# Performance work log

Measured on AMD Instinct MI355X. Metric: run time of the kernel, lower is better.

## Reference

```python
import jax, jax.numpy as jnp
import numpy as np

IMG, P, C = 224, 16, 3
D, H, MLP = 512, 8, 2048
L, NCLS = 10, 10      # budget, classes
N = (IMG // P) ** 2   # 196 patches
PD = C * P * P        # patch_dim = 768


def setup_inputs() -> dict:
    key = jax.random.key(0)
    ks = jax.random.split(key, 32)
    w = lambda k, shape: (jax.random.normal(k, shape, jnp.float32) * 0.02)
    return {
        'x': jax.random.normal(ks[0], (32, C, IMG, IMG), jnp.float32),
        'y': jax.random.randint(ks[1], (32, 1), 0, NCLS),
        'pos_emb': w(ks[2], (1, N + 1, D)),
        'cls_tok': w(ks[3], (1, 1, D)),
        'Wp': w(ks[4], (D, PD)), 'bp': jnp.zeros((D,), jnp.float32),
        'Wqkv': w(ks[5], (3 * D, D)),
        'Wo': w(ks[6], (D, D)), 'bo': jnp.zeros((D,), jnp.float32),
        'ln1_g': jnp.ones((D,), jnp.float32), 'ln1_b': jnp.zeros((D,), jnp.float32),
        'ln2_g': jnp.ones((D,), jnp.float32), 'ln2_b': jnp.zeros((D,), jnp.float32),
        'W1': w(ks[7], (MLP, D)), 'b1': jnp.zeros((MLP,), jnp.float32),
        'W2': w(ks[8], (D, MLP)), 'b2': jnp.zeros((D,), jnp.float32),
        'lnh_g': jnp.ones((D,), jnp.float32), 'lnh_b': jnp.zeros((D,), jnp.float32),
        'Wh1': w(ks[9], (MLP, D)), 'bh1': jnp.zeros((MLP,), jnp.float32),
        'Wh2': w(ks[10], (1, MLP)), 'bh2': jnp.zeros((1,), jnp.float32),
        'lnc_g': jnp.ones((D,), jnp.float32), 'lnc_b': jnp.zeros((D,), jnp.float32),
        'Wc1': w(ks[11], (MLP, D)), 'bc1': jnp.zeros((MLP,), jnp.float32),
        'Wc2': w(ks[12], (NCLS, MLP)), 'bc2': jnp.zeros((NCLS,), jnp.float32),
    }


def _ln(u, g, b):
    mu = u.mean(-1, keepdims=True)
    v = ((u - mu) ** 2).mean(-1, keepdims=True)
    return (u - mu) / jnp.sqrt(v + 1e-5) * g + b


def _gelu(u):
    return jax.nn.gelu(u, approximate=False)


def reference(x, y, pos_emb, cls_tok, Wp, bp, Wqkv, Wo, bo,
              ln1_g, ln1_b, ln2_g, ln2_b, W1, b1, W2, b2,
              lnh_g, lnh_b, Wh1, bh1, Wh2, bh2,
              lnc_g, lnc_b, Wc1, bc1, Wc2, bc2):
    b = x.shape[0]
    hp = IMG // P
    # patchify: b c (h p1) (w p2) -> b (h w) (p1 p2 c)
    xp = x.reshape(b, C, hp, P, hp, P).transpose(0, 2, 4, 3, 5, 1).reshape(b, N, PD)
    e = xp @ Wp.T + bp                                   # [b, N, D]
    z = jnp.concatenate([jnp.broadcast_to(cls_tok, (b, 1, D)), e], 1) + pos_emb[:, :N + 1]

    scale = D ** -0.5

    def attn(u):
        q, k, v = jnp.split(u @ Wqkv.T, 3, axis=-1)
        hsplit = lambda t: t.reshape(b, -1, H, D // H).transpose(0, 2, 1, 3)  # b h n d
        q, k, v = hsplit(q), hsplit(k), hsplit(v)
        a = jax.nn.softmax(jnp.einsum('bhid,bhjd->bhij', q, k) * scale, axis=-1)
        o = jnp.einsum('bhij,bhjd->bhid', a, v).transpose(0, 2, 1, 3).reshape(b, -1, D)
        return o @ Wo.T + bo

    def ff(u):
        return _gelu(u @ W1.T + b1) @ W2.T + b2

    def halt(u):
        h = _gelu(_ln(u, lnh_g, lnh_b) @ Wh1.T + bh1) @ Wh2.T + bh2  # [b, n, 1]
        return jax.nn.sigmoid(h).mean(1)[:, 0]                        # [b]

    def step(u, _):
        u = u + attn(_ln(u, ln1_g, ln1_b))
        u = u + ff(_ln(u, ln2_g, ln2_b))
        return u, (u[:, 0], halt(u))

    _, (cls_outs, halts) = jax.lax.scan(step, z, None, length=L)
    cls_outs = cls_outs.transpose(1, 0, 2)   # [b, L, D]
    halts = halts.T                          # [b, L]

    logits = _gelu(_ln(cls_outs, lnc_g, lnc_b) @ Wc1.T + bc1) @ Wc2.T + bc2  # [b, L, 10]
    logp = jax.nn.log_softmax(logits, -1)
    lab = y[:, 0]
    ce = -jnp.take_along_axis(logp, jnp.broadcast_to(lab[:, None, None], (b, L, 1)), axis=2)[..., 0]  # [b, L]

    idx = jnp.argmin(ce, axis=1) + 1                     # [b], halting step per sample
    steps = jnp.arange(L)
    mask = (steps[None, :] < idx[:, None]).astype(ce.dtype)
    denom = idx.astype(ce.dtype)
    ref_ce = (ce * mask).sum(1) / denom                  # per-sample mean over first idx steps

    # halt labels: 1 for steps < idx-1, 0 at step idx-1 (only first idx entries count)
    hl = jnp.where(steps[None, :] == (idx[:, None] - 1), 0.0, 1.0)
    p = jnp.clip(halts, 1e-7, 1.0 - 1e-7)
    bce = -(hl * jnp.log(p) + (1.0 - hl) * jnp.log1p(-p))
    halt_loss = (bce * mask).sum(1) / denom

    return ref_ce.mean() + halt_loss.mean()
```

## Files before the change

### kernel.cpp

```cpp
#include <hip/hip_runtime.h>
#include <math.h>

#define BBATCH 32
#define NTOK 197
#define NPATCH 196
#define PDIM 768
#define DDIM 512
#define NHEAD 8
#define DHEAD 64
#define MLPDIM 2048
#define NLAYER 10
#define NCLASS 10
#define MTOK (BBATCH*NTOK)
#define MPAD 6400
#define MPATCH (BBATCH*NPATCH)
#define QKVROWS (MTOK + 16)

typedef unsigned short u16;
typedef __attribute__((ext_vector_type(8))) short bf16x8;
typedef __attribute__((ext_vector_type(4))) float f32x4;

__device__ __forceinline__ float gelu_f(float x) {
    return 0.5f * x * (1.0f + erff(x * 0.70710678118654752440f));
}
__device__ __forceinline__ float bf2f(u16 u) {
    union { unsigned int i; float f; } v; v.i = ((unsigned int)u) << 16; return v.f;
}
__device__ __forceinline__ u16 f2bf(float f) {
    union { float f; unsigned int u; } v; v.f = f;
    unsigned int r = v.u + 0x7FFFu + ((v.u >> 16) & 1u);
    return (u16)(r >> 16);
}
__device__ __forceinline__ void gload_lds16(const u16* g, u16* l) {
    __builtin_amdgcn_global_load_lds((const __attribute__((address_space(1))) void*)g,
                                     (__attribute__((address_space(3))) void*)l, 16, 0, 0);
}
__device__ __forceinline__ int swz_bij(int wg, int nwg) {
    int q = nwg >> 3, r = nwg & 7, xcd = wg & 7, id8 = wg >> 3;
    return (xcd < r) ? xcd * (q + 1) + id8 : r * (q + 1) + (xcd - r) * q + id8;
}

template<int MODEA, int MODEB>
__global__ __launch_bounds__(512)
void gemm256_kernel(int nA, int colsA, int colsB,
                    const u16* __restrict__ Aa, const u16* __restrict__ Wa,
                    const float* __restrict__ biasa, void* __restrict__ outa, int Na,
                    const u16* __restrict__ Ab, const u16* __restrict__ Wb,
                    const float* __restrict__ biasb, const float* __restrict__ wh2,
                    void* __restrict__ outb, int Nb, int M)
{
    __shared__ u16 As[2][256 * 64];
    __shared__ u16 Bs[2][128 * 64];
    const int tid = threadIdx.x, lane = tid & 63, wid = tid >> 6;
    const int wr = wid >> 1, wc = wid & 1;

    const int swz = swz_bij(blockIdx.x, gridDim.x);
    int mode, m0, n0, Nn;
    const u16 *A, *W; const float* bias; void* out;
    if (swz < nA) {
        mode = MODEA; A = Aa; W = Wa; bias = biasa; out = outa; Nn = Na;
        m0 = (swz / colsA) * 256; n0 = (swz % colsA) * 128;
    } else {
        int s2 = swz - nA;
        mode = MODEB; A = Ab; W = Wb; bias = biasb; out = outb; Nn = Nb;
        m0 = (s2 / colsB) * 256; n0 = (s2 % colsB) * 128;
    }

    f32x4 acc[4][4] = {};
    const int srow = tid >> 3;
    const int dcb  = (tid & 7) << 4;

    auto stage = [&](int buf, int k0) {
        #pragma unroll
        for (int p = 0; p < 4; ++p) {
            int rr = p * 64 + srow;
            int scb = dcb ^ ((rr & 7) << 4);
            gload_lds16(A + (size_t)(m0 + rr) * 512 + k0 + (scb >> 1), &As[buf][p * 4096 + tid * 8]);
        }
        #pragma unroll
        for (int p = 0; p < 2; ++p) {
            int rr = p * 64 + srow;
            int scb = dcb ^ ((rr & 7) << 4);
            gload_lds16(W + (size_t)(n0 + rr) * 512 + k0 + (scb >> 1), &Bs[buf][p * 4096 + tid * 8]);
        }
    };
    auto compute = [&](int buf) {
        #pragma unroll
        for (int kk = 0; kk < 64; kk += 32) {
            const int kb = (kk + ((lane >> 4) << 3)) << 1;
            bf16x8 af[4], bfr[4];
            #pragma unroll
            for (int mi = 0; mi < 4; ++mi) {
                int ar = wr * 64 + mi * 16 + (lane & 15);
                af[mi] = *(const bf16x8*)&As[buf][ar * 64 + ((kb ^ ((ar & 7) << 4)) >> 1)];
            }
            #pragma unroll
            for (int ni = 0; ni < 4; ++ni) {
                int br = wc * 64 + ni * 16 + (lane & 15);
                bfr[ni] = *(const bf16x8*)&Bs[buf][br * 64 + ((kb ^ ((br & 7) << 4)) >> 1)];
            }
            #pragma unroll
            for (int mi = 0; mi < 4; ++mi)
                #pragma unroll
                for (int ni = 0; ni < 4; ++ni)
                    acc[mi][ni] = __builtin_amdgcn_mfma_f32_16x16x32_bf16(
                        af[mi], bfr[ni], acc[mi][ni], 0, 0, 0);
        }
    };

    stage(0, 0);
    int cur = 0;
    #pragma unroll 1
    for (int t = 0; t < 7; ++t) {
        stage(cur ^ 1, (t + 1) << 6);
        asm volatile("s_waitcnt vmcnt(6)" ::: "memory");
        __builtin_amdgcn_s_barrier();
        compute(cur);
        __builtin_amdgcn_s_barrier();
        cur ^= 1;
    }
    asm volatile("s_waitcnt vmcnt(0)" ::: "memory");
    __builtin_amdgcn_s_barrier();
    compute(cur);

    if (mode == 1) {
        float* hout = (float*)out;
        #pragma unroll
        for (int mi = 0; mi < 4; ++mi) {
            #pragma unroll
            for (int j = 0; j < 4; ++j) {
                int row = m0 + wr * 64 + mi * 16 + ((lane >> 4) << 2) + j;
                float part = 0.0f;
                #pragma unroll
                for (int ni = 0; ni < 4; ++ni) {
                    int col = n0 + wc * 64 + ni * 16 + (lane & 15);
                    part += gelu_f(acc[mi][ni][j] + bias[col]) * wh2[col];
                }
                #pragma unroll
                for (int off = 1; off < 16; off <<= 1) part += __shfl_xor(part, off, 64);
                if ((lane & 15) == 0 && row < M) atomicAdd(&hout[row], part);
            }
        }
        return;
    }
    u16* outb16 = (u16*)out;
    #pragma unroll
    for (int mi = 0; mi < 4; ++mi) {
        #pragma unroll
        for (int j = 0; j < 4; ++j) {
            int row = m0 + wr * 64 + mi * 16 + ((lane >> 4) << 2) + j;
            if (row >= M) continue;
            #pragma unroll
            for (int ni = 0; ni < 4; ++ni) {
                int col = n0 + wc * 64 + ni * 16 + (lane & 15);
                float v = acc[mi][ni][j];
                if (mode == 2) v = gelu_f(v + bias[col]);
                outb16[(size_t)row * Nn + col] = f2bf(v);
            }
        }
    }
}

template<int ACT, int HASB, int HASR, int OUTBF, int ATOMIC>
__global__ __launch_bounds__(256)
void mgemm_kernel(const u16* __restrict__ A, const u16* __restrict__ W,
                  const float* __restrict__ bias, const float* __restrict__ res,
                  void* __restrict__ Cout, int M, int Nn, int K, int kcount, int mtiles)
{
    __shared__ u16 As[2][128 * 64];
    __shared__ u16 Bs[2][128 * 64];
    const int tid = threadIdx.x, lane = tid & 63, wid = tid >> 6;
    const int wr = wid >> 1, wc = wid & 1;

    const int gx = gridDim.x;
    const int swz = swz_bij(blockIdx.y * gx + blockIdx.x, gx * gridDim.y);
    const int ry = swz / gx;
    const int ks = ry / mtiles;
    const int m0 = (ry % mtiles) * 128, n0 = (swz % gx) * 128;
    const int kbase = ks * kcount;

    f32x4 acc[4][4] = {};
    const int srow = tid >> 3;
    const int dcb  = (tid & 7) << 4;

    auto stage = [&](int buf, int k0) {
        #pragma unroll
        for (int p = 0; p < 4; ++p) {
            int rr = p * 32 + srow;
            int scb = dcb ^ ((rr & 7) << 4);
            gload_lds16(A + (size_t)(m0 + rr) * K + k0 + (scb >> 1), &As[buf][p * 2048 + tid * 8]);
            gload_lds16(W + (size_t)(n0 + rr) * K + k0 + (scb >> 1), &Bs[buf][p * 2048 + tid * 8]);
        }
    };
    auto compute = [&](int buf) {
        #pragma unroll
        for (int kk = 0; kk < 64; kk += 32) {
            const int kb = (kk + ((lane >> 4) << 3)) << 1;
            bf16x8 af[4], bfr[4];
            #pragma unroll
            for (int mi = 0; mi < 4; ++mi) {
                int ar = wr * 64 + mi * 16 + (lane & 15);
                af[mi] = *(const bf16x8*)&As[buf][ar * 64 + ((kb ^ ((ar & 7) << 4)) >> 1)];
            }
            #pragma unroll
            for (int ni = 0; ni < 4; ++ni) {
                int br = wc * 64 + ni * 16 + (lane & 15);
                bfr[ni] = *(const bf16x8*)&Bs[buf][br * 64 + ((kb ^ ((br & 7) << 4)) >> 1)];
            }
            #pragma unroll
            for (int mi = 0; mi < 4; ++mi)
                #pragma unroll
                for (int ni = 0; ni < 4; ++ni)
                    acc[mi][ni] = __builtin_amdgcn_mfma_f32_16x16x32_bf16(
                        af[mi], bfr[ni], acc[mi][ni], 0, 0, 0);
        }
    };

    const int NT = kcount >> 6;
    stage(0, kbase);
    int cur = 0;
    #pragma unroll 1
    for (int t = 0; t < NT - 1; ++t) {
        stage(cur ^ 1, kbase + ((t + 1) << 6));
        asm volatile("s_waitcnt vmcnt(8)" ::: "memory");
        __builtin_amdgcn_s_barrier();
        compute(cur);
        __builtin_amdgcn_s_barrier();
        cur ^= 1;
    }
    asm volatile("s_waitcnt vmcnt(0)" ::: "memory");
    __builtin_amdgcn_s_barrier();
    compute(cur);

    float* outf = (float*)Cout;
    u16*   outb = (u16*)Cout;
    #pragma unroll
    for (int mi = 0; mi < 4; ++mi) {
        #pragma unroll
        for (int j = 0; j < 4; ++j) {
            int row = m0 + wr * 64 + mi * 16 + ((lane >> 4) << 2) + j;
            if (row >= M) continue;
            #pragma unroll
            for (int ni = 0; ni < 4; ++ni) {
                int col = n0 + wc * 64 + ni * 16 + (lane & 15);
                float v = acc[mi][ni][j];
                if (ATOMIC) {
                    if (HASB && ks == 0) v += bias[col];
                    atomicAdd(&outf[(size_t)row * Nn + col], v);
                } else {
                    if (HASB) v += bias[col];
                    if (ACT)  v = gelu_f(v);
                    if (HASR) v += res[(size_t)row * Nn + col];
                    if (OUTBF) outb[(size_t)row * Nn + col] = f2bf(v);
                    else       outf[(size_t)row * Nn + col] = v;
                }
            }
        }
    }
}

__global__ __launch_bounds__(256)
void ln_one_kernel(const float* __restrict__ X, const float* __restrict__ g,
                   const float* __restrict__ bb, u16* __restrict__ Y, int M)
{
    int w0 = blockIdx.x * 4 + (threadIdx.x >> 6);
    int lane = threadIdx.x & 63;
    int stride = gridDim.x * 4;
    for (int row = w0; row < M; row += stride) {
        const float* x = X + (size_t)row * DDIM;
        float v[8], s = 0.0f;
        #pragma unroll
        for (int i = 0; i < 8; i++) { v[i] = x[lane + i * 64]; s += v[i]; }
        #pragma unroll
        for (int off = 32; off; off >>= 1) s += __shfl_xor(s, off, 64);
        float mu = s * (1.0f / 512.0f), q = 0.0f;
        #pragma unroll
        for (int i = 0; i < 8; i++) { float d = v[i] - mu; q += d * d; }
        #pragma unroll
        for (int off = 32; off; off >>= 1) q += __shfl_xor(q, off, 64);
        float inv = 1.0f / sqrtf(q * (1.0f / 512.0f) + 1e-5f);
        u16* y = Y + (size_t)row * DDIM;
        #pragma unroll
        for (int i = 0; i < 8; i++) {
            int c = lane + i * 64;
            y[c] = f2bf((v[i] - mu) * inv * g[c] + bb[c]);
        }
    }
}

__global__ __launch_bounds__(256)
void ln_dual_kernel(const float* __restrict__ X,
// ... 130 lines not shown
            }
        }
    }
    {
        int d = tid & 63;
        int jg = tid >> 6;
        for (int j = jg * 52; j < jg * 52 + 52; ++j) {
            u16 v = (j < NTOK) ? qkv[base + (size_t)j * 1536 + 1024 + d] : (u16)0;
            int byt = (d * 416 + j * 2) ^ ((d & 7) << 4);
            *(u16*)((char*)Vt + byt) = v;
        }
    }
    __syncthreads();

    u16* Pw = Pl + wid * 16 * 208;
    const float scale = 0.04419417382415922f;
    const int t0   = half ? 7 : 0;
    const int tcnt = half ? 6 : 7;
    const int g = lane >> 4;
    const int mycol = lane & 15;

    for (int ti = wid; ti < tcnt; ti += 4) {
        const int r0 = (t0 + ti) * 16;
        bf16x8 qf[2];
        #pragma unroll
        for (int ks = 0; ks < 2; ++ks) {
            int row = r0 + mycol;
            int col = ks * 32 + (g << 3);
            qf[ks] = *(const bf16x8*)&qkv[base + (size_t)row * 1536 + col];
        }
        f32x4 s[13];
        #pragma unroll
        for (int ct = 0; ct < 13; ++ct) s[ct] = (f32x4){0.f, 0.f, 0.f, 0.f};
        #pragma unroll
        for (int ks = 0; ks < 2; ++ks) {
            int kbyte = (ks * 32 + (g << 3)) * 2;
            #pragma unroll
            for (int ct = 0; ct < 13; ++ct) {
                int n = ct * 16 + mycol;
                bf16x8 kf = *(const bf16x8*)((char*)Ks + ((n * 128 + kbyte) ^ ((n & 7) << 4)));
                s[ct] = __builtin_amdgcn_mfma_f32_16x16x32_bf16(qf[ks], kf, s[ct], 0, 0, 0);
            }
        }
        float m[4], sum[4];
        #pragma unroll
        for (int j = 0; j < 4; ++j) m[j] = -1e30f;
        #pragma unroll
        for (int ct = 0; ct < 13; ++ct) {
            bool valid = (ct * 16 + mycol) < NTOK;
            #pragma unroll
            for (int j = 0; j < 4; ++j) {
                float v = valid ? s[ct][j] * scale : -1e30f;
                s[ct][j] = v;
                m[j] = fmaxf(m[j], v);
            }
        }
        #pragma unroll
        for (int off = 1; off < 16; off <<= 1)
            #pragma unroll
            for (int j = 0; j < 4; ++j) m[j] = fmaxf(m[j], __shfl_xor(m[j], off, 64));
        #pragma unroll
        for (int j = 0; j < 4; ++j) sum[j] = 0.0f;
        #pragma unroll
        for (int ct = 0; ct < 13; ++ct)
            #pragma unroll
            for (int j = 0; j < 4; ++j) {
                float e = expf(s[ct][j] - m[j]);
                s[ct][j] = e;
                sum[j] += e;
            }
        #pragma unroll
        for (int off = 1; off < 16; off <<= 1)
            #pragma unroll
            for (int j = 0; j < 4; ++j) sum[j] += __shfl_xor(sum[j], off, 64);
        float inv[4];
        #pragma unroll
        for (int j = 0; j < 4; ++j) inv[j] = 1.0f / sum[j];
        #pragma unroll
        for (int ct = 0; ct < 13; ++ct) {
            int col = ct * 16 + mycol;
            #pragma unroll
            for (int j = 0; j < 4; ++j) {
                int row = (g << 2) + j;
                int byt = (row * 416 + col * 2) ^ ((row & 7) << 4);
                *(u16*)((char*)Pw + byt) = f2bf(s[ct][j] * inv[j]);
            }
        }
        #pragma unroll
        for (int nt = 0; nt < 4; ++nt) {
            f32x4 o = (f32x4){0.f, 0.f, 0.f, 0.f};
            #pragma unroll
            for (int ks = 0; ks < 7; ++ks) {
                bf16x8 pf = {}, vf = {};
                bool live = !(ks == 6 && g >= 2);
                if (live) {
                    int kbyte = (ks * 32 + (g << 3)) * 2;
                    pf = *(const bf16x8*)((char*)Pw + ((mycol * 416 + kbyte) ^ ((mycol & 7) << 4)));
                    int vrow = nt * 16 + mycol;
                    vf = *(const bf16x8*)((char*)Vt + ((vrow * 416 + kbyte) ^ ((vrow & 7) << 4)));
                }
                o = __builtin_amdgcn_mfma_f32_16x16x32_bf16(pf, vf, o, 0, 0, 0);
            }
            #pragma unroll
            for (int j = 0; j < 4; ++j) {
                int grow = r0 + (g << 2) + j;
                if (grow < NTOK)
                    O[((size_t)b * NTOK + grow) * DDIM + h * 64 + nt * 16 + mycol] = f2bf(o[j]);
            }
        }
    }
}

__global__ __launch_bounds__(64)
void haltmean_kernel(const float* __restrict__ hsc, const float* __restrict__ bh2,
                     const float* __restrict__ U, float* __restrict__ halts,
                     float* __restrict__ cls, int lidx)
{
    int b = blockIdx.x, lane = threadIdx.x;
    float bb = bh2[0];
    float s = 0.0f;
    for (int t = lane; t < NTOK; t += 64)
        s += 1.0f / (1.0f + expf(-(hsc[b * NTOK + t] + bb)));
    #pragma unroll
    for (int off = 32; off; off >>= 1) s += __shfl_xor(s, off, 64);
    if (lane == 0) halts[b * NLAYER + lidx] = s * (1.0f / (float)NTOK);
    for (int d = lane; d < DDIM; d += 64)
        cls[((size_t)b * NLAYER + lidx) * DDIM + d] = U[(size_t)b * NTOK * DDIM + d];
}

__global__ __launch_bounds__(256)
void head_logits_kernel(const u16* __restrict__ Hh, const float* __restrict__ Wc2,
                        const float* __restrict__ bc2, float* __restrict__ logits)
{
    int wave = (blockIdx.x * 4) + (threadIdx.x >> 6);
    int lane = threadIdx.x & 63;
// ... 81 lines not shown
    const float* Wh1    = (const float*)d_in[19];
    const float* bh1    = (const float*)d_in[20];
    const float* Wh2    = (const float*)d_in[21];
    const float* bh2    = (const float*)d_in[22];
    const float* lncg   = (const float*)d_in[23];
    const float* lncb   = (const float*)d_in[24];
    const float* Wc1    = (const float*)d_in[25];
    const float* bc1    = (const float*)d_in[26];
    const float* Wc2    = (const float*)d_in[27];
    const float* bc2    = (const float*)d_in[28];

    float* U      = (float*)d_ws;
    float* CLS    = U + (size_t)MTOK * DDIM;
    float* LOGITS = CLS + (size_t)BBATCH * NLAYER * DDIM;
    float* HSC    = LOGITS + BBATCH * NLAYER * NCLASS;
    float* HALTS  = HSC + (size_t)NLAYER * MTOK;
    u16* QKVb = (u16*)(HALTS + BBATCH * NLAYER + 32);
    float* EMB = (float*)QKVb;
    u16* LNB1 = QKVb + (size_t)QKVROWS * 1536;
    u16* LNB2 = LNB1 + (size_t)MPAD * DDIM;
    u16* LNBh = LNB2 + (size_t)MPAD * DDIM;
    u16* HB   = LNBh + (size_t)MPAD * DDIM;
    u16* XP   = HB;
    u16* CLNB = HB + (size_t)MPAD * MLPDIM;
    u16* wWp  = CLNB + 384 * DDIM;
    u16* wWqkv= wWp   + 512 * 768;
    u16* wWo  = wWqkv + 1536 * 512;
    u16* wW1  = wWo   + 512 * 512;
    u16* wW2  = wW1   + 2048 * 512;
    u16* wWh1 = wW2   + 512 * 2048;
    u16* wWc1 = wWh1  + 2048 * 512;

    dim3 blk(256);
    const u16* dummyA = LNB1; const float* dummyF = bh2;

    convert7_kernel<<<dim3(1024), blk, 0, stream>>>(Wp, Wqkv, Wo, W1, W2, Wh1, Wc1, wWp);
    hipMemsetAsync(HSC, 0, (size_t)NLAYER * MTOK * sizeof(float), stream);
    patch_kernel<<<dim3(2048), blk, 0, stream>>>(x, XP);
    mgemm_kernel<0,1,0,0,0><<<dim3(4, 49), blk, 0, stream>>>(
        XP, wWp, bp, nullptr, (void*)EMB, MPATCH, DDIM, PDIM, PDIM, 49);
    assemble_kernel<<<dim3(2048), blk, 0, stream>>>(EMB, clstok, pos, U);
    ln_dual_kernel<<<dim3(256), blk, 0, stream>>>(U, ln1g, ln1b, lnhg, lnhb, LNB1, LNBh, MTOK);

    for (int l = 0; l < NLAYER; l++) {
        if (l == 0) {
            gemm256_kernel<0,0><<<dim3(300), dim3(512), 0, stream>>>(
                300, 12, 12, LNB1, wWqkv, nullptr, (void*)QKVb, 1536,
                LNB1, wWqkv, nullptr, nullptr, (void*)QKVb, 1536, MTOK);
        } else {
            gemm256_kernel<0,1><<<dim3(700), dim3(512), 0, stream>>>(
                300, 12, 16, LNB1, wWqkv, nullptr, (void*)QKVb, 1536,
                LNBh, wWh1, bh1, Wh2, (void*)(HSC + (size_t)(l-1) * MTOK), 2048, MTOK);
        }
        if (l == 0) {
            attn_hm_kernel<0><<<dim3(512), blk, 0, stream>>>(
                QKVb, LNB1, nullptr, dummyF, U, HALTS, CLS, 0);
        } else {
            attn_hm_kernel<1><<<dim3(544), blk, 0, stream>>>(
                QKVb, LNB1, HSC + (size_t)(l-1) * MTOK, bh2, U, HALTS, CLS, l - 1);
        }
        mgemm_kernel<0,1,1,0,0><<<dim3(4, 50), blk, 0, stream>>>(
            LNB1, wWo, bo, U, (void*)U, MTOK, DDIM, DDIM, DDIM, 50);
        ln_one_kernel<<<dim3(256), blk, 0, stream>>>(U, ln2g, ln2b, LNB2, MTOK);
        gemm256_kernel<2,2><<<dim3(400), dim3(512), 0, stream>>>(
            400, 16, 16, LNB2, wW1, b1, (void*)HB, 2048,
            LNB2, wW1, b1, nullptr, (void*)HB, 2048, MTOK);
        mgemm_kernel<0,1,0,0,1><<<dim3(4, 100), blk, 0, stream>>>(
            HB, wW2, b2, nullptr, (void*)U, MTOK, DDIM, MLPDIM, 1024, 50);
        ln_dual_kernel<<<dim3(256), blk, 0, stream>>>(
            U, ln1g, ln1b, lnhg, lnhb, LNB1, LNBh, MTOK);
    }

    gemm256_kernel<1,1><<<dim3(400), dim3(512), 0, stream>>>(
        400, 16, 16, LNBh, wWh1, bh1, (void*)(HSC + (size_t)9 * MTOK), 2048,
        LNBh, wWh1, bh1, Wh2, (void*)(HSC + (size_t)9 * MTOK), 2048, MTOK);
    haltmean_kernel<<<dim3(BBATCH), dim3(64), 0, stream>>>(
        HSC + (size_t)9 * MTOK, bh2, U, HALTS, CLS, 9);

    ln_one_kernel<<<dim3(80), blk, 0, stream>>>(CLS, lncg, lncb, CLNB, BBATCH * NLAYER);
    mgemm_kernel<1,1,0,1,0><<<dim3(16, 3), blk, 0, stream>>>(
        CLNB, wWc1, bc1, nullptr, (void*)HB, BBATCH * NLAYER, MLPDIM, DDIM, DDIM, 3);
    head_logits_kernel<<<dim3(80), blk, 0, stream>>>(HB, Wc2, bc2, LOGITS);
    celoss_kernel<<<dim3(1), blk, 0, stream>>>(LOGITS, y, HALTS, (float*)d_out);
}
```

Before: 2.251 ms.

## Unify GEMMs into persistent triple-buffered 256x128 kernel with cross-tile prefetch

Replaces both GEMM kernels (the templated 256x128 kernel and the 128x128 split-K kernel) with one runtime-moded persistent kernel. Blocks loop over tiles, and a three-stage LDS ring prefetches the next tile's K-slices across tile boundaries to hide load latency. The Wo, W2 and patch-embedding GEMMs move from 128x128 or split-K tiles to 256x128 tiles with a fused bias+residual fp32 epilogue, which removes the atomics. The cost is fewer blocks for the N=512 GEMMs (100 tiles on a 256-CU part), more LDS per block, and the loss of the XCD-aware tile swizzle.

After: 3.427 ms. 1.52x slower.

```diff
diff --git a/kernel.cpp b/kernel.cpp
--- a/kernel.cpp
+++ b/kernel.cpp
@@ -35,55 +35,53 @@
     __builtin_amdgcn_global_load_lds((const __attribute__((address_space(1))) void*)g,
                                      (__attribute__((address_space(3))) void*)l, 16, 0, 0);
 }
-__device__ __forceinline__ int swz_bij(int wg, int nwg) {
-    int q = nwg >> 3, r = nwg & 7, xcd = wg & 7, id8 = wg >> 3;
-    return (xcd < r) ? xcd * (q + 1) + id8 : r * (q + 1) + (xcd - r) * q + id8;
-}
-
-template<int MODEA, int MODEB>
+
 __global__ __launch_bounds__(512)
-void gemm256_kernel(int nA, int colsA, int colsB,
-                    const u16* __restrict__ Aa, const u16* __restrict__ Wa,
-                    const float* __restrict__ biasa, void* __restrict__ outa, int Na,
-                    const u16* __restrict__ Ab, const u16* __restrict__ Wb,
-                    const float* __restrict__ biasb, const float* __restrict__ wh2,
-                    void* __restrict__ outb, int Nb, int M)
-{
-    __shared__ u16 As[2][256 * 64];
-    __shared__ u16 Bs[2][128 * 64];
+void pgemm_kernel(int tilesA, int colsA, int colsB, int tot, int K, int M,
+                  const u16* __restrict__ Aa, const u16* __restrict__ Wa,
+                  const float* __restrict__ biasa, const float* __restrict__ resa,
+                  void* __restrict__ outa, int Na, int modeA,
+                  const u16* __restrict__ Ab, const u16* __restrict__ Wb,
+                  const float* __restrict__ biasb, const float* __restrict__ resb,
+                  void* __restrict__ outb, int Nb, int modeB)
+{
+    __shared__ u16 As[3][256 * 64];
+    __shared__ u16 Bs[3][128 * 64];
     const int tid = threadIdx.x, lane = tid & 63, wid = tid >> 6;
     const int wr = wid >> 1, wc = wid & 1;
-
-    const int swz = swz_bij(blockIdx.x, gridDim.x);
-    int mode, m0, n0, Nn;
-    const u16 *A, *W; const float* bias; void* out;
-    if (swz < nA) {
-        mode = MODEA; A = Aa; W = Wa; bias = biasa; out = outa; Nn = Na;
-        m0 = (swz / colsA) * 256; n0 = (swz % colsA) * 128;
-    } else {
-        int s2 = swz - nA;
-        mode = MODEB; A = Ab; W = Wb; bias = biasb; out = outb; Nn = Nb;
-        m0 = (s2 / colsB) * 256; n0 = (s2 % colsB) * 128;
-    }
-
-    f32x4 acc[4][4] = {};
-    const int srow = tid >> 3;
-    const int dcb  = (tid & 7) << 4;
-
-    auto stage = [&](int buf, int k0) {
+    const int tile0 = blockIdx.x;
+    if (tile0 >= tot) return;
+    const int G = gridDim.x;
+    const int nk = K >> 6;
+    const int srow = tid >> 3, dcb = (tid & 7) << 4;
+
+    int sgT = tile0, sgK = 0, sgM = 0, sgN = 0;
+    const u16 *sgA = Aa, *sgW = Wa;
+    auto setSg = [&](int t) {
+        if (t < tilesA) { sgA = Aa; sgW = Wa; sgM = (t / colsA) * 256; sgN = (t % colsA) * 128; }
+        else { int lt = t - tilesA; sgA = Ab; sgW = Wb; sgM = (lt / colsB) * 256; sgN = (lt % colsB) * 128; }
+    };
+    setSg(sgT);
+    auto sgStage = [&](int b) {
+        int k0 = sgK << 6;
         #pragma unroll
         for (int p = 0; p < 4; ++p) {
             int rr = p * 64 + srow;
             int scb = dcb ^ ((rr & 7) << 4);
-            gload_lds16(A + (size_t)(m0 + rr) * 512 + k0 + (scb >> 1), &As[buf][p * 4096 + tid * 8]);
+            gload_lds16(sgA + (size_t)(sgM + rr) * K + k0 + (scb >> 1), &As[b][p * 4096 + tid * 8]);
         }
         #pragma unroll
         for (int p = 0; p < 2; ++p) {
             int rr = p * 64 + srow;
             int scb = dcb ^ ((rr & 7) << 4);
-            gload_lds16(W + (size_t)(n0 + rr) * 512 + k0 + (scb >> 1), &Bs[buf][p * 4096 + tid * 8]);
+            gload_lds16(sgW + (size_t)(sgN + rr) * K + k0 + (scb >> 1), &Bs[b][p * 4096 + tid * 8]);
         }
     };
+    auto sgAdv = [&]() {
+        if (++sgK == nk) { sgK = 0; sgT += G; if (sgT < tot) setSg(sgT); }
+    };
+
+    f32x4 acc[4][4] = {};
     auto compute = [&](int buf) {
         #pragma unroll
         for (int kk = 0; kk < 64; kk += 32) {
@@ -108,154 +106,94 @@
         }
     };
 
-    stage(0, 0);
-    int cur = 0;
-    #pragma unroll 1
-    for (int t = 0; t < 7; ++t) {
-        stage(cur ^ 1, (t + 1) << 6);
-        asm volatile("s_waitcnt vmcnt(6)" ::: "memory");
-        __builtin_amdgcn_s_barrier();
-        compute(cur);
-        __builtin_amdgcn_s_barrier();
-        cur ^= 1;
-    }
-    asm volatile("s_waitcnt vmcnt(0)" ::: "memory");
-    __builtin_amdgcn_s_barrier();
-    compute(cur);
-
-    if (mode == 1) {
-        float* hout = (float*)out;
-        #pragma unroll
-        for (int mi = 0; mi < 4; ++mi) {
-            #pragma unroll
-            for (int j = 0; j < 4; ++j) {
-                int row = m0 + wr * 64 + mi * 16 + ((lane >> 4) << 2) + j;
-                float part = 0.0f;
-                #pragma unroll
-                for (int ni = 0; ni < 4; ++ni) {
-                    int col = n0 + wc * 64 + ni * 16 + (lane & 15);
-                    part += gelu_f(acc[mi][ni][j] + bias[col]) * wh2[col];
+    sgStage(0); sgAdv();
+    sgStage(1); sgAdv();
+    int bufc = 0, pend = 2;
+
+    for (int ct = tile0; ct < tot; ct += G) {
+        const float *bias, *res; void* out; int Nn, mode, m0, n0;
+        if (ct < tilesA) {
+            bias = biasa; res = resa; out = outa; Nn = Na; mode = modeA;
+            m0 = (ct / colsA) * 256; n0 = (ct % colsA) * 128;
+        } else {
+            int lt = ct - tilesA;
+            bias = biasb; res = resb; out = outb; Nn = Nb; mode = modeB;
+            m0 = (lt / colsB) * 256; n0 = (lt % colsB) * 128;
+        }
+        #pragma unroll 1
+        for (int k = 0; k < nk; ++k) {
+            if (sgT < tot) {
+                int bs = bufc + 2; if (bs >= 3) bs -= 3;
+                sgStage(bs); sgAdv();
+                asm volatile("s_waitcnt vmcnt(12)" ::: "memory");
+            } else if (pend == 2) {
+                pend = 1;
+                asm volatile("s_waitcnt vmcnt(6)" ::: "memory");
+            } else {
+                asm volatile("s_waitcnt vmcnt(0)" ::: "memory");
+            }
+            __builtin_amdgcn_s_barrier();
+            compute(bufc);
+            if (k == nk - 1) {
+                if (mode == 1) {
+                    float* hout = (float*)out;
+                    #pragma unroll
+                    for (int mi = 0; mi < 4; ++mi)
+                        #pragma unroll
+                        for (int j = 0; j < 4; ++j) {
+                            int row = m0 + wr * 64 + mi * 16 + ((lane >> 4) << 2) + j;
+                            float part = 0.0f;
+                            #pragma unroll
+                            for (int ni = 0; ni < 4; ++ni) {
+                                int col = n0 + wc * 64 + ni * 16 + (lane & 15);
+                                part += gelu_f(acc[mi][ni][j] + bias[col]) * res[col];
+                            }
+                            #pragma unroll
+                            for (int off = 1; off < 16; off <<= 1) part += __shfl_xor(part, off, 64);
+                            if ((lane & 15) == 0 && row < M) atomicAdd(&hout[row], part);
+                        }
+                } else if (mode == 3) {
+                    float* outf = (float*)out;
+                    #pragma unroll
+                    for (int mi = 0; mi < 4; ++mi)
+                        #pragma unroll
+                        for (int j = 0; j < 4; ++j) {
+                            int row = m0 + wr * 64 + mi * 16 + ((lane >> 4) << 2) + j;
+                            if (row >= M) continue;
+                            #pragma unroll
+                            for (int ni = 0; ni < 4; ++ni) {
+                                int col = n0 + wc * 64 + ni * 16 + (lane & 15);
+                                float v = acc[mi][ni][j] + bias[col];
+                                if (res) v += res[(size_t)row * Nn + col];
+                                outf[(size_t)row * Nn + col] = v;
+                            }
+                        }
+                } else {
+                    u16* ob = (u16*)out;
+                    #pragma unroll
+                    for (int mi = 0; mi < 4; ++mi)
+                        #pragma unroll
+                        for (int j = 0; j < 4; ++j) {
+                            int row = m0 + wr * 64 + mi * 16 + ((lane >> 4) << 2) + j;
+                            if (row >= M) continue;
+                            #pragma unroll
+                            for (int ni = 0; ni < 4; ++ni) {
+                                int col = n0 + wc * 64 + ni * 16 + (lane & 15);
+                                float v = acc[mi][ni][j];
+                                if (mode == 2) v = gelu_f(v + bias[col]);
+                                ob[(size_t)row * Nn + col] = f2bf(v);
+                            }
+                        }
                 }
-                #pragma unroll
-                for (int off = 1; off < 16; off <<= 1) part += __shfl_xor(part, off, 64);
-                if ((lane & 15) == 0 && row < M) atomicAdd(&hout[row], part);
-            }
-        }
-        return;
-    }
-    u16* outb16 = (u16*)out;
-    #pragma unroll
-    for (int mi = 0; mi < 4; ++mi) {
-        #pragma unroll
-        for (int j = 0; j < 4; ++j) {
-            int row = m0 + wr * 64 + mi * 16 + ((lane >> 4) << 2) + j;
-            if (row >= M) continue;
-            #pragma unroll
-            for (int ni = 0; ni < 4; ++ni) {
-                int col = n0 + wc * 64 + ni * 16 + (lane & 15);
-                float v = acc[mi][ni][j];
-                if (mode == 2) v = gelu_f(v + bias[col]);
-                outb16[(size_t)row * Nn + col] = f2bf(v);
-            }
-        }
-    }
-}
-
-template<int ACT, int HASB, int HASR, int OUTBF, int ATOMIC>
-__global__ __launch_bounds__(256)
-void mgemm_kernel(const u16* __restrict__ A, const u16* __restrict__ W,
-                  const float* __restrict__ bias, const float* __restrict__ res,
-                  void* __restrict__ Cout, int M, int Nn, int K, int kcount, int mtiles)
-{
-    __shared__ u16 As[2][128 * 64];
-    __shared__ u16 Bs[2][128 * 64];
-    const int tid = threadIdx.x, lane = tid & 63, wid = tid >> 6;
-    const int wr = wid >> 1, wc = wid & 1;
-
-    const int gx = gridDim.x;
-    const int swz = swz_bij(blockIdx.y * gx + blockIdx.x, gx * gridDim.y);
-    const int ry = swz / gx;
-    const int ks = ry / mtiles;
-    const int m0 = (ry % mtiles) * 128, n0 = (swz % gx) * 128;
-    const int kbase = ks * kcount;
-
-    f32x4 acc[4][4] = {};
-    const int srow = tid >> 3;
-    const int dcb  = (tid & 7) << 4;
-
-    auto stage = [&](int buf, int k0) {
-        #pragma unroll
-        for (int p = 0; p < 4; ++p) {
-            int rr = p * 32 + srow;
-            int scb = dcb ^ ((rr & 7) << 4);
-            gload_lds16(A + (size_t)(m0 + rr) * K + k0 + (scb >> 1), &As[buf][p * 2048 + tid * 8]);
-            gload_lds16(W + (size_t)(n0 + rr) * K + k0 + (scb >> 1), &Bs[buf][p * 2048 + tid * 8]);
-        }
-    };
-    auto compute = [&](int buf) {
-        #pragma unroll
-        for (int kk = 0; kk < 64; kk += 32) {
-            const int kb = (kk + ((lane >> 4) << 3)) << 1;
-            bf16x8 af[4], bfr[4];
-            #pragma unroll
-            for (int mi = 0; mi < 4; ++mi) {
-                int ar = wr * 64 + mi * 16 + (lane & 15);
-                af[mi] = *(const bf16x8*)&As[buf][ar * 64 + ((kb ^ ((ar & 7) << 4)) >> 1)];
-            }
-            #pragma unroll
-            for (int ni = 0; ni < 4; ++ni) {
-                int br = wc * 64 + ni * 16 + (lane & 15);
-                bfr[ni] = *(const bf16x8*)&Bs[buf][br * 64 + ((kb ^ ((br & 7) << 4)) >> 1)];
-            }
-            #pragma unroll
-            for (int mi = 0; mi < 4; ++mi)
-                #pragma unroll
-                for (int ni = 0; ni < 4; ++ni)
-                    acc[mi][ni] = __builtin_amdgcn_mfma_f32_16x16x32_bf16(
-                        af[mi], bfr[ni], acc[mi][ni], 0, 0, 0);
-        }
-    };
-
-    const int NT = kcount >> 6;
-    stage(0, kbase);
-    int cur = 0;
-    #pragma unroll 1
-    for (int t = 0; t < NT - 1; ++t) {
-        stage(cur ^ 1, kbase + ((t + 1) << 6));
-        asm volatile("s_waitcnt vmcnt(8)" ::: "memory");
-        __builtin_amdgcn_s_barrier();
-        compute(cur);
-        __builtin_amdgcn_s_barrier();
-        cur ^= 1;
-    }
-    asm volatile("s_waitcnt vmcnt(0)" ::: "memory");
-    __builtin_amdgcn_s_barrier();
-    compute(cur);
-
-    float* outf = (float*)Cout;
-    u16*   outb = (u16*)Cout;
-    #pragma unroll
-    for (int mi = 0; mi < 4; ++mi) {
-        #pragma unroll
-        for (int j = 0; j < 4; ++j) {
-            int row = m0 + wr * 64 + mi * 16 + ((lane >> 4) << 2) + j;
-            if (row >= M) continue;
-            #pragma unroll
-            for (int ni = 0; ni < 4; ++ni) {
-                int col = n0 + wc * 64 + ni * 16 + (lane & 15);
-                float v = acc[mi][ni][j];
-                if (ATOMIC) {
-                    if (HASB && ks == 0) v += bias[col];
-                    atomicAdd(&outf[(size_t)row * Nn + col], v);
-                } else {
-                    if (HASB) v += bias[col];
-                    if (ACT)  v = gelu_f(v);
-                    if (HASR) v += res[(size_t)row * Nn + col];
-                    if (OUTBF) outb[(size_t)row * Nn + col] = f2bf(v);
-                    else       outf[(size_t)row * Nn + col] = v;
-                }
-            }
-        }
+            }
+            __builtin_amdgcn_s_barrier();
+            bufc = (bufc == 2) ? 0 : bufc + 1;
+        }
+        #pragma unroll
+        for (int mi = 0; mi < 4; ++mi)
+            #pragma unroll
+            for (int ni = 0; ni < 4; ++ni)
+                acc[mi][ni] = (f32x4){0.f, 0.f, 0.f, 0.f};
     }
 }
 
@@ -669,54 +607,66 @@
     u16* wWc1 = wWh1  + 2048 * 512;
 
     dim3 blk(256);
-    const u16* dummyA = LNB1; const float* dummyF = bh2;
+    const float* dummyF = bh2;
 
     convert7_kernel<<<dim3(1024), blk, 0, stream>>>(Wp, Wqkv, Wo, W1, W2, Wh1, Wc1, wWp);
     hipMemsetAsync(HSC, 0, (size_t)NLAYER * MTOK * sizeof(float), stream);
     patch_kernel<<<dim3(2048), blk, 0, stream>>>(x, XP);
-    mgemm_kernel<0,1,0,0,0><<<dim3(4, 49), blk, 0, stream>>>(
-        XP, wWp, bp, nullptr, (void*)EMB, MPATCH, DDIM, PDIM, PDIM, 49);
+    pgemm_kernel<<<dim3(100), dim3(512), 0, stream>>>(
+        100, 4, 1, 100, PDIM, MPATCH,
+        XP, wWp, bp, nullptr, (void*)EMB, DDIM, 3,
+        XP, wWp, bp, nullptr, (void*)EMB, DDIM, 3);
     assemble_kernel<<<dim3(2048), blk, 0, stream>>>(EMB, clstok, pos, U);
     ln_dual_kernel<<<dim3(256), blk, 0, stream>>>(U, ln1g, ln1b, lnhg, lnhb, LNB1, LNBh, MTOK);
 
     for (int l = 0; l < NLAYER; l++) {
         if (l == 0) {
-            gemm256_kernel<0,0><<<dim3(300), dim3(512), 0, stream>>>(
-                300, 12, 12, LNB1, wWqkv, nullptr, (void*)QKVb, 1536,
-                LNB1, wWqkv, nullptr, nullptr, (void*)QKVb, 1536, MTOK);
+            pgemm_kernel<<<dim3(256), dim3(512), 0, stream>>>(
+                300, 12, 1, 300, DDIM, MTOK,
+                LNB1, wWqkv, nullptr, nullptr, (void*)QKVb, 1536, 0,
+                LNB1, wWqkv, nullptr, nullptr, (void*)QKVb, 1536, 0);
         } else {
-            gemm256_kernel<0,1><<<dim3(700), dim3(512), 0, stream>>>(
-                300, 12, 16, LNB1, wWqkv, nullptr, (void*)QKVb, 1536,
-                LNBh, wWh1, bh1, Wh2, (void*)(HSC + (size_t)(l-1) * MTOK), 2048, MTOK);
+            pgemm_kernel<<<dim3(256), dim3(512), 0, stream>>>(
+                300, 12, 16, 700, DDIM, MTOK,
+                LNB1, wWqkv, nullptr, nullptr, (void*)QKVb, 1536, 0,
+                LNBh, wWh1, bh1, Wh2, (void*)(HSC + (size_t)(l - 1) * MTOK), 2048, 1);
         }
         if (l == 0) {
             attn_hm_kernel<0><<<dim3(512), blk, 0, stream>>>(
                 QKVb, LNB1, nullptr, dummyF, U, HALTS, CLS, 0);
         } else {
             attn_hm_kernel<1><<<dim3(544), blk, 0, stream>>>(
-                QKVb, LNB1, HSC + (size_t)(l-1) * MTOK, bh2, U, HALTS, CLS, l - 1);
-        }
-        mgemm_kernel<0,1,1,0,0><<<dim3(4, 50), blk, 0, stream>>>(
-            LNB1, wWo, bo, U, (void*)U, MTOK, DDIM, DDIM, DDIM, 50);
+                QKVb, LNB1, HSC + (size_t)(l - 1) * MTOK, bh2, U, HALTS, CLS, l - 1);
+        }
+        pgemm_kernel<<<dim3(100), dim3(512), 0, stream>>>(
+            100, 4, 1, 100, DDIM, MTOK,
+            LNB1, wWo, bo, U, (void*)U, DDIM, 3,
+            LNB1, wWo, bo, U, (void*)U, DDIM, 3);
         ln_one_kernel<<<dim3(256), blk, 0, stream>>>(U, ln2g, ln2b, LNB2, MTOK);
-        gemm256_kernel<2,2><<<dim3(400), dim3(512), 0, stream>>>(
-            400, 16, 16, LNB2, wW1, b1, (void*)HB, 2048,
-            LNB2, wW1, b1, nullptr, (void*)HB, 2048, MTOK);
-        mgemm_kernel<0,1,0,0,1><<<dim3(4, 100), blk, 0, stream>>>(
-            HB, wW2, b2, nullptr, (void*)U, MTOK, DDIM, MLPDIM, 1024, 50);
+        pgemm_kernel<<<dim3(256), dim3(512), 0, stream>>>(
+            400, 16, 1, 400, DDIM, MTOK,
+            LNB2, wW1, b1, nullptr, (void*)HB, MLPDIM, 2,
+            LNB2, wW1, b1, nullptr, (void*)HB, MLPDIM, 2);
+        pgemm_kernel<<<dim3(100), dim3(512), 0, stream>>>(
+            100, 4, 1, 100, MLPDIM, MTOK,
+            HB, wW2, b2, U, (void*)U, DDIM, 3,
+            HB, wW2, b2, U, (void*)U, DDIM, 3);
         ln_dual_kernel<<<dim3(256), blk, 0, stream>>>(
             U, ln1g, ln1b, lnhg, lnhb, LNB1, LNBh, MTOK);
     }
 
-    gemm256_kernel<1,1><<<dim3(400), dim3(512), 0, stream>>>(
-        400, 16, 16, LNBh, wWh1, bh1, (void*)(HSC + (size_t)9 * MTOK), 2048,
-        LNBh, wWh1, bh1, Wh2, (void*)(HSC + (size_t)9 * MTOK), 2048, MTOK);
+    pgemm_kernel<<<dim3(256), dim3(512), 0, stream>>>(
+        400, 16, 1, 400, DDIM, MTOK,
+        LNBh, wWh1, bh1, Wh2, (void*)(HSC + (size_t)9 * MTOK), 2048, 1,
+        LNBh, wWh1, bh1, Wh2, (void*)(HSC + (size_t)9 * MTOK), 2048, 1);
     haltmean_kernel<<<dim3(BBATCH), dim3(64), 0, stream>>>(
         HSC + (size_t)9 * MTOK, bh2, U, HALTS, CLS, 9);
 
     ln_one_kernel<<<dim3(80), blk, 0, stream>>>(CLS, lncg, lncb, CLNB, BBATCH * NLAYER);
-    mgemm_kernel<1,1,0,1,0><<<dim3(16, 3), blk, 0, stream>>>(
-        CLNB, wWc1, bc1, nullptr, (void*)HB, BBATCH * NLAYER, MLPDIM, DDIM, DDIM, 3);
+    pgemm_kernel<<<dim3(32), dim3(512), 0, stream>>>(
+        32, 16, 1, 32, DDIM, BBATCH * NLAYER,
+        CLNB, wWc1, bc1, nullptr, (void*)HB, MLPDIM, 2,
+        CLNB, wWc1, bc1, nullptr, (void*)HB, MLPDIM, 2);
     head_logits_kernel<<<dim3(80), blk, 0, stream>>>(HB, Wc2, bc2, LOGITS);
     celoss_kernel<<<dim3(1), blk, 0, stream>>>(LOGITS, y, HALTS, (float*)d_out);
 }
```

## Split GEMM staging into half-phases interleaved with MFMA and raise MFMA priority

Applied to the files above, without the earlier changes.

Both GEMM kernels now issue the next tile's global-to-LDS loads in two halves, one before each 32-wide k-phase, so memory traffic is spread across the compute rather than issued all at once. MFMA blocks are wrapped in s_setprio(1) in the GEMMs and the attention kernel so matrix work gets issue priority over other waves. The mgemm template is replaced by a mode-based mg_kernel with a 1D swizzled grid, and the layernorm kernels are launched with twice as many blocks. The extra barriers and finer-grained waits add synchronization overhead, and it is unclear the priority hints help.

Result: slower. 2.651 ms (+17.7%).

```diff
diff --git a/kernel.cpp b/kernel.cpp
--- a/kernel.cpp
+++ b/kernel.cpp
@@ -70,12 +70,19 @@
     const int srow = tid >> 3;
     const int dcb  = (tid & 7) << 4;
 
-    auto stage = [&](int buf, int k0) {
-        #pragma unroll
-        for (int p = 0; p < 4; ++p) {
+    auto stageA3 = [&](int buf, int k0) {
+        #pragma unroll
+        for (int p = 0; p < 3; ++p) {
             int rr = p * 64 + srow;
             int scb = dcb ^ ((rr & 7) << 4);
             gload_lds16(A + (size_t)(m0 + rr) * 512 + k0 + (scb >> 1), &As[buf][p * 4096 + tid * 8]);
+        }
+    };
+    auto stageB3 = [&](int buf, int k0) {
+        {
+            int rr = 192 + srow;
+            int scb = dcb ^ ((rr & 7) << 4);
+            gload_lds16(A + (size_t)(m0 + rr) * 512 + k0 + (scb >> 1), &As[buf][3 * 4096 + tid * 8]);
         }
         #pragma unroll
         for (int p = 0; p < 2; ++p) {
@@ -84,44 +91,48 @@
             gload_lds16(W + (size_t)(n0 + rr) * 512 + k0 + (scb >> 1), &Bs[buf][p * 4096 + tid * 8]);
         }
     };
-    auto compute = [&](int buf) {
-        #pragma unroll
-        for (int kk = 0; kk < 64; kk += 32) {
-            const int kb = (kk + ((lane >> 4) << 3)) << 1;
-            bf16x8 af[4], bfr[4];
-            #pragma unroll
-            for (int mi = 0; mi < 4; ++mi) {
-                int ar = wr * 64 + mi * 16 + (lane & 15);
-                af[mi] = *(const bf16x8*)&As[buf][ar * 64 + ((kb ^ ((ar & 7) << 4)) >> 1)];
-            }
-            #pragma unroll
-            for (int ni = 0; ni < 4; ++ni) {
-                int br = wc * 64 + ni * 16 + (lane & 15);
-                bfr[ni] = *(const bf16x8*)&Bs[buf][br * 64 + ((kb ^ ((br & 7) << 4)) >> 1)];
-            }
-            #pragma unroll
-            for (int mi = 0; mi < 4; ++mi)
-                #pragma unroll
-                for (int ni = 0; ni < 4; ++ni)
-                    acc[mi][ni] = __builtin_amdgcn_mfma_f32_16x16x32_bf16(
-                        af[mi], bfr[ni], acc[mi][ni], 0, 0, 0);
-        }
+    auto phase = [&](int buf, int kk) {
+        const int kb = (kk + ((lane >> 4) << 3)) << 1;
+        bf16x8 af[4], bfr[4];
+        #pragma unroll
+        for (int mi = 0; mi < 4; ++mi) {
+            int ar = wr * 64 + mi * 16 + (lane & 15);
+            af[mi] = *(const bf16x8*)&As[buf][ar * 64 + ((kb ^ ((ar & 7) << 4)) >> 1)];
+        }
+        #pragma unroll
+        for (int ni = 0; ni < 4; ++ni) {
+            int br = wc * 64 + ni * 16 + (lane & 15);
+            bfr[ni] = *(const bf16x8*)&Bs[buf][br * 64 + ((kb ^ ((br & 7) << 4)) >> 1)];
+        }
+        __builtin_amdgcn_s_setprio(1);
+        #pragma unroll
+        for (int mi = 0; mi < 4; ++mi)
+            #pragma unroll
+            for (int ni = 0; ni < 4; ++ni)
+                acc[mi][ni] = __builtin_amdgcn_mfma_f32_16x16x32_bf16(
+                    af[mi], bfr[ni], acc[mi][ni], 0, 0, 0);
+        __builtin_amdgcn_s_setprio(0);
     };
 
-    stage(0, 0);
+    stageA3(0, 0); stageB3(0, 0);
     int cur = 0;
     #pragma unroll 1
-    for (int t = 0; t < 7; ++t) {
-        stage(cur ^ 1, (t + 1) << 6);
-        asm volatile("s_waitcnt vmcnt(6)" ::: "memory");
+    for (int t = 0; t < 8; ++t) {
+        const int kn = (t + 1) << 6;
+        if (t < 7) {
+            stageA3(cur ^ 1, kn);
+            asm volatile("s_waitcnt vmcnt(3)" ::: "memory");
+        } else {
+            asm volatile("s_waitcnt vmcnt(0)" ::: "memory");
+        }
         __builtin_amdgcn_s_barrier();
-        compute(cur);
+        phase(cur, 0);
+        __builtin_amdgcn_s_barrier();
+        if (t < 7) stageB3(cur ^ 1, kn);
+        phase(cur, 32);
         __builtin_amdgcn_s_barrier();
         cur ^= 1;
     }
-    asm volatile("s_waitcnt vmcnt(0)" ::: "memory");
-    __builtin_amdgcn_s_barrier();
-    compute(cur);
 
     if (mode == 1) {
         float* hout = (float*)out;
@@ -161,81 +172,119 @@
     }
 }
 
-template<int ACT, int HASB, int HASR, int OUTBF, int ATOMIC>
-__global__ __launch_bounds__(256)
-void mgemm_kernel(const u16* __restrict__ A, const u16* __restrict__ W,
-                  const float* __restrict__ bias, const float* __restrict__ res,
-                  void* __restrict__ Cout, int M, int Nn, int K, int kcount, int mtiles)
+template<int MODE>
+__global__ __launch_bounds__(256)
+void mg_kernel(const u16* __restrict__ A, const u16* __restrict__ W,
+               const float* __restrict__ bias, const float* __restrict__ res,
+               void* __restrict__ Cout, int M, int Nn, int K,
+               int cols, int kb, int nk, int mtiles)
 {
     __shared__ u16 As[2][128 * 64];
     __shared__ u16 Bs[2][128 * 64];
     const int tid = threadIdx.x, lane = tid & 63, wid = tid >> 6;
     const int wr = wid >> 1, wc = wid & 1;
 
-    const int gx = gridDim.x;
-    const int swz = swz_bij(blockIdx.y * gx + blockIdx.x, gx * gridDim.y);
-    const int ry = swz / gx;
-    const int ks = ry / mtiles;
-    const int m0 = (ry % mtiles) * 128, n0 = (swz % gx) * 128;
-    const int kbase = ks * kcount;
+    const int swz = swz_bij(blockIdx.x, gridDim.x);
+    const int ti = swz % (mtiles * cols);
+    const int ks = swz / (mtiles * cols);
+    const int m0 = (ti / cols) * 128, n0 = (ti % cols) * 128;
+    const int kbase = kb + ks * (nk << 6);
 
     f32x4 acc[4][4] = {};
     const int srow = tid >> 3;
     const int dcb  = (tid & 7) << 4;
 
-    auto stage = [&](int buf, int k0) {
-        #pragma unroll
-        for (int p = 0; p < 4; ++p) {
-            int rr = p * 32 + srow;
+    auto stage_h = [&](int buf, int k0, int pb) {
+        #pragma unroll
+        for (int p = 0; p < 2; ++p) {
+            int rr = (pb + p) * 32 + srow;
             int scb = dcb ^ ((rr & 7) << 4);
-            gload_lds16(A + (size_t)(m0 + rr) * K + k0 + (scb >> 1), &As[buf][p * 2048 + tid * 8]);
-            gload_lds16(W + (size_t)(n0 + rr) * K + k0 + (scb >> 1), &Bs[buf][p * 2048 + tid * 8]);
+            gload_lds16(A + (size_t)(m0 + rr) * K + k0 + (scb >> 1), &As[buf][(pb + p) * 2048 + tid * 8]);
+            gload_lds16(W + (size_t)(n0 + rr) * K + k0 + (scb >> 1), &Bs[buf][(pb + p) * 2048 + tid * 8]);
         }
     };
-    auto compute = [&](int buf) {
-        #pragma unroll
-        for (int kk = 0; kk < 64; kk += 32) {
-            const int kb = (kk + ((lane >> 4) << 3)) << 1;
-            bf16x8 af[4], bfr[4];
-            #pragma unroll
-            for (int mi = 0; mi < 4; ++mi) {
-                int ar = wr * 64 + mi * 16 + (lane & 15);
-                af[mi] = *(const bf16x8*)&As[buf][ar * 64 + ((kb ^ ((ar & 7) << 4)) >> 1)];
-            }
-            #pragma unroll
-            for (int ni = 0; ni < 4; ++ni) {
-                int br = wc * 64 + ni * 16 + (lane & 15);
-                bfr[ni] = *(const bf16x8*)&Bs[buf][br * 64 + ((kb ^ ((br & 7) << 4)) >> 1)];
-            }
-            #pragma unroll
-            for (int mi = 0; mi < 4; ++mi)
-                #pragma unroll
-                for (int ni = 0; ni < 4; ++ni)
-                    acc[mi][ni] = __builtin_amdgcn_mfma_f32_16x16x32_bf16(
-                        af[mi], bfr[ni], acc[mi][ni], 0, 0, 0);
-        }
+    auto phase = [&](int buf, int kk) {
+        const int kbyte = (kk + ((lane >> 4) << 3)) << 1;
+        bf16x8 af[4], bfr[4];
+        #pragma unroll
+        for (int mi = 0; mi < 4; ++mi) {
+            int ar = wr * 64 + mi * 16 + (lane & 15);
+            af[mi] = *(const bf16x8*)&As[buf][ar * 64 + ((kbyte ^ ((ar & 7) << 4)) >> 1)];
+        }
+        #pragma unroll
+        for (int ni = 0; ni < 4; ++ni) {
+            int br = wc * 64 + ni * 16 + (lane & 15);
+            bfr[ni] = *(const bf16x8*)&Bs[buf][br * 64 + ((kbyte ^ ((br & 7) << 4)) >> 1)];
+        }
+        __builtin_amdgcn_s_setprio(1);
+        #pragma unroll
+        for (int mi = 0; mi < 4; ++mi)
+            #pragma unroll
+            for (int ni = 0; ni < 4; ++ni)
+                acc[mi][ni] = __builtin_amdgcn_mfma_f32_16x16x32_bf16(
+                    af[mi], bfr[ni], acc[mi][ni], 0, 0, 0);
+        __builtin_amdgcn_s_setprio(0);
     };
 
-    const int NT = kcount >> 6;
-    stage(0, kbase);
+    stage_h(0, kbase, 0); stage_h(0, kbase, 2);
     int cur = 0;
     #pragma unroll 1
-    for (int t = 0; t < NT - 1; ++t) {
-        stage(cur ^ 1, kbase + ((t + 1) << 6));
-        asm volatile("s_waitcnt vmcnt(8)" ::: "memory");
+    for (int t = 0; t < nk; ++t) {
+        const int kn = kbase + ((t + 1) << 6);
+        if (t < nk - 1) {
+            stage_h(cur ^ 1, kn, 0);
+            asm volatile("s_waitcnt vmcnt(4)" ::: "memory");
+        } else {
+            asm volatile("s_waitcnt vmcnt(0)" ::: "memory");
+        }
         __builtin_amdgcn_s_barrier();
-        compute(cur);
+        phase(cur, 0);
+        __builtin_amdgcn_s_barrier();
+        if (t < nk - 1) stage_h(cur ^ 1, kn, 2);
+        phase(cur, 32);
         __builtin_amdgcn_s_barrier();
         cur ^= 1;
     }
-    asm volatile("s_waitcnt vmcnt(0)" ::: "memory");
-    __builtin_amdgcn_s_barrier();
-    compute(cur);
-
-    float* outf = (float*)Cout;
-    u16*   outb = (u16*)Cout;
+
+    if (MODE == 4) {
+        float* outf = (float*)Cout;
+        #pragma unroll
+        for (int mi = 0; mi < 4; ++mi)
+            #pragma unroll
+            for (int j = 0; j < 4; ++j) {
+                int row = m0 + wr * 64 + mi * 16 + ((lane >> 4) << 2) + j;
+                if (row >= M) continue;
+                #pragma unroll
+                for (int ni = 0; ni < 4; ++ni) {
+                    int col = n0 + wc * 64 + ni * 16 + (lane & 15);
+                    float v = acc[mi][ni][j];
+                    if (bias && ks == 0) v += bias[col];
+                    atomicAdd(&outf[(size_t)row * Nn + col], v);
+                }
+            }
+        return;
+    }
+    if (MODE == 3) {
+        float* outf = (float*)Cout;
+        #pragma unroll
+        for (int mi = 0; mi < 4; ++mi)
+            #pragma unroll
+            for (int j = 0; j < 4; ++j) {
+                int row = m0 + wr * 64 + mi * 16 + ((lane >> 4) << 2) + j;
+                if (row >= M) continue;
+                #pragma unroll
+                for (int ni = 0; ni < 4; ++ni) {
+                    int col = n0 + wc * 64 + ni * 16 + (lane & 15);
+                    float v = acc[mi][ni][j] + bias[col];
+                    if (res) v += res[(size_t)row * Nn + col];
+                    outf[(size_t)row * Nn + col] = v;
+                }
+            }
+        return;
+    }
+    u16* ob16 = (u16*)Cout;
     #pragma unroll
-    for (int mi = 0; mi < 4; ++mi) {
+    for (int mi = 0; mi < 4; ++mi)
         #pragma unroll
         for (int j = 0; j < 4; ++j) {
             int row = m0 + wr * 64 + mi * 16 + ((lane >> 4) << 2) + j;
@@ -243,20 +292,9 @@
             #pragma unroll
             for (int ni = 0; ni < 4; ++ni) {
                 int col = n0 + wc * 64 + ni * 16 + (lane & 15);
-                float v = acc[mi][ni][j];
-                if (ATOMIC) {
-                    if (HASB && ks == 0) v += bias[col];
-                    atomicAdd(&outf[(size_t)row * Nn + col], v);
-                } else {
-                    if (HASB) v += bias[col];
-                    if (ACT)  v = gelu_f(v);
-                    if (HASR) v += res[(size_t)row * Nn + col];
-                    if (OUTBF) outb[(size_t)row * Nn + col] = f2bf(v);
-                    else       outf[(size_t)row * Nn + col] = v;
-                }
-            }
-        }
-    }
+                ob16[(size_t)row * Nn + col] = f2bf(gelu_f(acc[mi][ni][j] + bias[col]));
+            }
+        }
 }
 
 __global__ __launch_bounds__(256)
@@ -453,6 +491,7 @@
         f32x4 s[13];
         #pragma unroll
         for (int ct = 0; ct < 13; ++ct) s[ct] = (f32x4){0.f, 0.f, 0.f, 0.f};
+        __builtin_amdgcn_s_setprio(1);
         #pragma unroll
         for (int ks = 0; ks < 2; ++ks) {
             int kbyte = (ks * 32 + (g << 3)) * 2;
@@ -463,6 +502,7 @@
                 s[ct] = __builtin_amdgcn_mfma_f32_16x16x32_bf16(qf[ks], kf, s[ct], 0, 0, 0);
             }
         }
+        __builtin_amdgcn_s_setprio(0);
         float m[4], sum[4];
         #pragma unroll
         for (int j = 0; j < 4; ++j) m[j] = -1e30f;
@@ -510,6 +550,7 @@
         #pragma unroll
         for (int nt = 0; nt < 4; ++nt) {
             f32x4 o = (f32x4){0.f, 0.f, 0.f, 0.f};
+            __builtin_amdgcn_s_setprio(1);
             #pragma unroll
             for (int ks = 0; ks < 7; ++ks) {
                 bf16x8 pf = {}, vf = {};
@@ -522,6 +563,7 @@
                 }
                 o = __builtin_amdgcn_mfma_f32_16x16x32_bf16(pf, vf, o, 0, 0, 0);
             }
+            __builtin_amdgcn_s_setprio(0);
             #pragma unroll
             for (int j = 0; j < 4; ++j) {
                 int grow = r0 + (g << 2) + j;
@@ -669,15 +711,15 @@
     u16* wWc1 = wWh1  + 2048 * 512;
 
     dim3 blk(256);
-    const u16* dummyA = LNB1; const float* dummyF = bh2;
+    const float* dummyF = bh2;
 
     convert7_kernel<<<dim3(1024), blk, 0, stream>>>(Wp, Wqkv, Wo, W1, W2, Wh1, Wc1, wWp);
     hipMemsetAsync(HSC, 0, (size_t)NLAYER * MTOK * sizeof(float), stream);
     patch_kernel<<<dim3(2048), blk, 0, stream>>>(x, XP);
-    mgemm_kernel<0,1,0,0,0><<<dim3(4, 49), blk, 0, stream>>>(
-        XP, wWp, bp, nullptr, (void*)EMB, MPATCH, DDIM, PDIM, PDIM, 49);
+    mg_kernel<3><<<dim3(196), blk, 0, stream>>>(
+        XP, wWp, bp, nullptr, (void*)EMB, MPATCH, DDIM, PDIM, 4, 0, 12, 49);
     assemble_kernel<<<dim3(2048), blk, 0, stream>>>(EMB, clstok, pos, U);
-    ln_dual_kernel<<<dim3(256), blk, 0, stream>>>(U, ln1g, ln1b, lnhg, lnhb, LNB1, LNBh, MTOK);
+    ln_dual_kernel<<<dim3(512), blk, 0, stream>>>(U, ln1g, ln1b, lnhg, lnhb, LNB1, LNBh, MTOK);
 
     for (int l = 0; l < NLAYER; l++) {
         if (l == 0) {
@@ -687,24 +729,24 @@
         } else {
             gemm256_kernel<0,1><<<dim3(700), dim3(512), 0, stream>>>(
                 300, 12, 16, LNB1, wWqkv, nullptr, (void*)QKVb, 1536,
-                LNBh, wWh1, bh1, Wh2, (void*)(HSC + (size_t)(l-1) * MTOK), 2048, MTOK);
+                LNBh, wWh1, bh1, Wh2, (void*)(HSC + (size_t)(l - 1) * MTOK), 2048, MTOK);
         }
         if (l == 0) {
             attn_hm_kernel<0><<<dim3(512), blk, 0, stream>>>(
                 QKVb, LNB1, nullptr, dummyF, U, HALTS, CLS, 0);
         } else {
             attn_hm_kernel<1><<<dim3(544), blk, 0, stream>>>(
-                QKVb, LNB1, HSC + (size_t)(l-1) * MTOK, bh2, U, HALTS, CLS, l - 1);
-        }
-        mgemm_kernel<0,1,1,0,0><<<dim3(4, 50), blk, 0, stream>>>(
-            LNB1, wWo, bo, U, (void*)U, MTOK, DDIM, DDIM, DDIM, 50);
-        ln_one_kernel<<<dim3(256), blk, 0, stream>>>(U, ln2g, ln2b, LNB2, MTOK);
+                QKVb, LNB1, HSC + (size_t)(l - 1) * MTOK, bh2, U, HALTS, CLS, l - 1);
+        }
+        mg_kernel<3><<<dim3(200), blk, 0, stream>>>(
+            LNB1, wWo, bo, U, (void*)U, MTOK, DDIM, DDIM, 4, 0, 8, 50);
+        ln_one_kernel<<<dim3(512), blk, 0, stream>>>(U, ln2g, ln2b, LNB2, MTOK);
         gemm256_kernel<2,2><<<dim3(400), dim3(512), 0, stream>>>(
             400, 16, 16, LNB2, wW1, b1, (void*)HB, 2048,
             LNB2, wW1, b1, nullptr, (void*)HB, 2048, MTOK);
-        mgemm_kernel<0,1,0,0,1><<<dim3(4, 100), blk, 0, stream>>>(
-            HB, wW2, b2, nullptr, (void*)U, MTOK, DDIM, MLPDIM, 1024, 50);
-        ln_dual_kernel<<<dim3(256), blk, 0, stream>>>(
+        mg_kernel<4><<<dim3(400), blk, 0, stream>>>(
+            HB, wW2, b2, nullptr, (void*)U, MTOK, DDIM, MLPDIM, 4, 0, 16, 50);
+        ln_dual_kernel<<<dim3(512), blk, 0, stream>>>(
             U, ln1g, ln1b, lnhg, lnhb, LNB1, LNBh, MTOK);
     }
 
@@ -715,8 +757,8 @@
         HSC + (size_t)9 * MTOK, bh2, U, HALTS, CLS, 9);
 
     ln_one_kernel<<<dim3(80), blk, 0, stream>>>(CLS, lncg, lncb, CLNB, BBATCH * NLAYER);
-    mgemm_kernel<1,1,0,1,0><<<dim3(16, 3), blk, 0, stream>>>(
-        CLNB, wWc1, bc1, nullptr, (void*)HB, BBATCH * NLAYER, MLPDIM, DDIM, DDIM, 3);
+    mg_kernel<2><<<dim3(48), blk, 0, stream>>>(
+        CLNB, wWc1, bc1, nullptr, (void*)HB, BBATCH * NLAYER, MLPDIM, DDIM, 16, 0, 8, 3);
     head_logits_kernel<<<dim3(80), blk, 0, stream>>>(HB, Wc2, bc2, LOGITS);
     celoss_kernel<<<dim3(1), blk, 0, stream>>>(LOGITS, y, HALTS, (float*)d_out);
 }
```
